# Performance work log

Measured on AMD Instinct MI355X. Metric: run time of the kernel, lower is better.

The kernel has to match this reference:

```python
import jax, jax.numpy as jnp
import numpy as np

H_HEADS = 16
D_K = 64
D_V = 64
D_MODEL = H_HEADS * D_K  # 1024
B, S = 2, 2048


def _xavier(key, shape):
    fan_in, fan_out = shape
    limit = float(np.sqrt(6.0 / (fan_in + fan_out)))
    return jax.random.uniform(key, shape, jnp.float32, -limit, limit)


def setup_inputs() -> dict:
    key = jax.random.key(0)
    ks = jax.random.split(key, 6)
    return {
        "batch": jax.random.normal(ks[0], (B, S, D_MODEL), jnp.float32),
        "attention_mask": jnp.zeros((S, S), jnp.float32),
        "W_Q": _xavier(ks[1], (D_MODEL, H_HEADS * D_K)),
        "W_K": _xavier(ks[2], (D_MODEL, H_HEADS * D_K)),
        "W_V": _xavier(ks[3], (D_MODEL, H_HEADS * D_V)),
        "b_Q": jnp.zeros((H_HEADS * D_K,), jnp.float32),
        "b_K": jnp.zeros((H_HEADS * D_K,), jnp.float32),
        "b_V": jnp.zeros((H_HEADS * D_V,), jnp.float32),
        "W_O": _xavier(ks[4], (H_HEADS * D_V, D_MODEL)),
        "b_O": jnp.zeros((D_MODEL,), jnp.float32),
    }


def reference(batch, attention_mask, W_Q, W_K, W_V, b_Q, b_K, b_V, W_O, b_O):
    # Batched equivalent of the per-head loop: project all heads at once,
    # then split the last dim into (h, d). Same math, one GEMM each.
    q = batch @ W_Q + b_Q  # [B,S,h*dk]
    k = batch @ W_K + b_K
    v = batch @ W_V + b_V
    q = q.reshape(B, S, H_HEADS, D_K)
    k = k.reshape(B, S, H_HEADS, D_K)
    v = v.reshape(B, S, H_HEADS, D_V)
    scale = 1.0 / jnp.sqrt(jnp.asarray(D_K, jnp.float32))
    scores = jnp.einsum("bqhd,bkhd->bhqk", q, k) * scale  # [B,h,S,S]
    scores = scores + attention_mask  # broadcast over batch & heads
    attn = jax.nn.softmax(scores, axis=-1)
    out = jnp.einsum("bhqk,bkhd->bqhd", attn, v)  # [B,S,h,dv]
    out = out.reshape(B, S, H_HEADS * D_V)  # concat over heads
    return out @ W_O + b_O
```

## Files before the change

kernel.cpp:

```cpp
#include <hip/hip_runtime.h>
#include <hip/hip_bf16.h>

typedef __attribute__((ext_vector_type(8))) short bf16x8;
typedef __attribute__((ext_vector_type(4))) float f32x4;
typedef __attribute__((ext_vector_type(4))) unsigned short u16x4;
typedef __attribute__((ext_vector_type(8))) unsigned short u16x8;

#define DEVI static __device__ __forceinline__

DEVI unsigned short f2bf(float f) {
  union { __hip_bfloat16 h; unsigned short u; } cv;
  cv.h = __float2bfloat16(f);
  return cv.u;
}

DEVI float bf2f(unsigned short u) {
  union { unsigned int i; float f; } cv;
  cv.i = (unsigned int)u << 16;
  return cv.f;
}

DEVI void gld_lds16(const unsigned short* g, unsigned short* l) {
  __builtin_amdgcn_global_load_lds(
      (const __attribute__((address_space(1))) unsigned int*)g,
      (__attribute__((address_space(3))) unsigned int*)l, 16, 0, 0);
}


__global__ void k_cvt_x(const float* __restrict__ x, unsigned short* __restrict__ xb) {
  int i = blockIdx.x * 256 + threadIdx.x;
  f32x4 v = *((const f32x4*)x + i);
  u16x4 o;
#pragma unroll
  for (int j = 0; j < 4; ++j) o[j] = f2bf(v[j]);
  *((u16x4*)xb + i) = o;
}

__global__ void k_wt(const float* __restrict__ Wq, const float* __restrict__ Wk,
                     const float* __restrict__ Wv, const float* __restrict__ Wo,
                     unsigned short* __restrict__ wqkvT, unsigned short* __restrict__ woT) {
  __shared__ float lt[32][33];
  int t = blockIdx.x;
  int g = t >> 10, r = t & 1023, kt = r >> 5, nt = r & 31;
  const float* W = (g == 0) ? Wq : (g == 1) ? Wk : (g == 2) ? Wv : Wo;
  unsigned short* out = (g < 3) ? (wqkvT + (size_t)g * 1024 * 1024) : woT;
  int tid = threadIdx.x;
  int row = tid >> 3, c4 = tid & 7;
  f32x4 v = *(const f32x4*)(W + (size_t)(kt * 32 + row) * 1024 + nt * 32 + c4 * 4);
#pragma unroll
  for (int j = 0; j < 4; ++j) lt[row][c4 * 4 + j] = v[j];
  __syncthreads();
  u16x4 o;
#pragma unroll
  for (int j = 0; j < 4; ++j) o[j] = f2bf(lt[c4 * 4 + j][row]);
  *(u16x4*)(out + (size_t)(nt * 32 + row) * 1024 + kt * 32 + c4 * 4) = o;
}

__global__ void k_bias(const float* __restrict__ bq, const float* __restrict__ bk,
                       const float* __restrict__ bv, float* __restrict__ bcat) {
  int i = blockIdx.x * 256 + threadIdx.x;
  if (i < 3072) bcat[i] = (i < 1024) ? bq[i] : (i < 2048) ? bk[i - 1024] : bv[i - 2048];
}

__global__ void k_mt(const float* __restrict__ mask, unsigned short* __restrict__ mU) {
  __shared__ float lt[32][33];
  int q0 = blockIdx.y * 32, k0 = blockIdx.x * 32;
  int tid = threadIdx.x;
  int row = tid >> 3, c4 = tid & 7;
  f32x4 v = *(const f32x4*)(mask + (size_t)(q0 + row) * 2048 + k0 + c4 * 4);
#pragma unroll
  for (int j = 0; j < 4; ++j) lt[row][c4 * 4 + j] = v[j] * 1.4426950408889634f;
  __syncthreads();
  int kq = tid >> 5, qr = tid & 31;
  u16x4 o;
#pragma unroll
  for (int j = 0; j < 4; ++j) o[j] = f2bf(lt[qr][kq * 4 + j]);
  *(u16x4*)(mU + ((size_t)(k0 >> 2) + kq) * 8192 + (size_t)(q0 + qr) * 4) = o;
}

__global__ void k_vt(const unsigned short* __restrict__ qkv, unsigned short* __restrict__ vt) {
  __shared__ unsigned short lt[64][72];
  int bh = blockIdx.y, s0 = blockIdx.x * 64;
  int b = bh >> 4, h = bh & 15;
  int tid = threadIdx.x;
#pragma unroll
  for (int i = 0; i < 2; ++i) {
    int c = tid + i * 256;
    int row = c >> 3, c8 = (c & 7) * 8;
    u16x8 v = *(const u16x8*)(qkv + (size_t)(b * 2048 + s0 + row) * 3072 + 2048 + h * 64 + c8);
#pragma unroll
    for (int j = 0; j < 8; ++j) lt[row][c8 + j] = v[j];
  }
  __syncthreads();
#pragma unroll
  for (int i = 0; i < 2; ++i) {
    int c = tid + i * 256;
    int d = c >> 3, s8 = (c & 7) * 8;
    u16x8 o;
#pragma unroll
    for (int j = 0; j < 8; ++j) o[j] = lt[s8 + j][d];
    *(u16x8*)(vt + (size_t)(bh * 64 + d) * 2048 + s0 + s8) = o;
  }
}

template <int OUT_BF16>
__launch_bounds__(256)
__global__ void k_gemm(const unsigned short* __restrict__ A,
                       const unsigned short* __restrict__ Bt,
                       const float* __restrict__ bias, void* __restrict__ C,
                       int M, int N, int K) {
  __shared__ unsigned short lA[128 * 32];
  __shared__ unsigned short lB[128 * 32];
  int tid = threadIdx.x;
  int m0 = blockIdx.y * 128, n0 = blockIdx.x * 128;
  int w = tid >> 6, l = tid & 63;
  int wm = (w >> 1) * 64, wn = (w & 1) * 64;
  int lg = l >> 4, lc = l & 15;
  f32x4 acc[4][4] = {};
  const unsigned short* Ab = A + (size_t)m0 * K;
  const unsigned short* Bb = Bt + (size_t)n0 * K;

  for (int kk = 0; kk < K; kk += 32) {
#pragma unroll
    for (int i = 0; i < 2; ++i) {
      int c = tid + i * 256;
      int row = c >> 2, c8 = (c & 3) * 8;
      gld_lds16(Ab + (size_t)row * K + kk + c8, lA + c * 8);
    }
#pragma unroll
    for (int i = 0; i < 2; ++i) {
      int c = tid + i * 256;
      int row = c >> 2, c8 = (c & 3) * 8;
      gld_lds16(Bb + (size_t)row * K + kk + c8, lB + c * 8);
    }
    __syncthreads();
    bf16x8 af[4], bfr[4];
#pragma unroll
    for (int mf = 0; mf < 4; ++mf)
      af[mf] = *(const bf16x8*)(lA + (wm + mf * 16 + lc) * 32 + lg * 8);
#pragma unroll
    for (int nf = 0; nf < 4; ++nf)
      bfr[nf] = *(const bf16x8*)(lB + (wn + nf * 16 + lc) * 32 + lg * 8);
#pragma unroll
    for (int mf = 0; mf < 4; ++mf)
#pragma unroll
      for (int nf = 0; nf < 4; ++nf)
        acc[mf][nf] = __builtin_amdgcn_mfma_f32_16x16x32_bf16(af[mf], bfr[nf], acc[mf][nf], 0, 0, 0);
    __syncthreads();
  }

  int lr = lg * 4;
  float bv[4];
#pragma unroll
  for (int nf = 0; nf < 4; ++nf) bv[nf] = bias[n0 + wn + nf * 16 + lc];
#pragma unroll
  for (int mf = 0; mf < 4; ++mf)
#pragma unroll
    for (int nf = 0; nf < 4; ++nf)
#pragma unroll
      for (int rr = 0; rr < 4; ++rr) {
        size_t gm = m0 + wm + mf * 16 + lr + rr;
        size_t gn = n0 + wn + nf * 16 + lc;
        float v = acc[mf][nf][rr] + bv[nf];
        if (OUT_BF16)
          ((unsigned short*)C)[gm * N + gn] = f2bf(v);
        else
          ((float*)C)[gm * N + gn] = v;
      }
}

__launch_bounds__(256, 4)
__global__ void k_attn(const unsigned short* __restrict__ qkv,
                       const unsigned short* __restrict__ vt,
                       const unsigned short* __restrict__ mU,
                       unsigned short* __restrict__ ao) {
  __shared__ unsigned short lK[2][64 * 64];
  __shared__ unsigned short lV[2][64 * 64];
  __shared__ unsigned short lP[64 * 64];
  int wg0 = blockIdx.x;
  int wg = (wg0 & 7) * 128 + (wg0 >> 3);
  int b = wg >> 9, r0 = wg & 511, h = r0 >> 5, qt = r0 & 31;
  int tid = threadIdx.x, w = tid >> 6, l = tid & 63;
  int lg = l >> 4, lc = l & 15;
  int c = lc & 7;
  int q0 = qt * 64 + w * 16;

  const unsigned short* Qb = qkv + (size_t)(b * 2048 + q0) * 3072 + h * 64;
  const unsigned short* Kb = qkv + (size_t)(b * 2048) * 3072 + 1024 + h * 64;
  const unsigned short* Vb = vt + (size_t)((b * 16 + h) * 64) * 2048;
  const unsigned short* mUb = mU + (size_t)lg * 8192 + (size_t)(q0 + lc) * 4;

  int rsub = l >> 3;
  int scol = ((l & 7) ^ rsub) * 8;

  bf16x8 qf[2];
#pragma unroll
  for (int ks = 0; ks < 2; ++ks)
    qf[ks] = *(const bf16x8*)(Qb + (size_t)lc * 3072 + ks * 32 + lg * 8);

  f32x4 o2[4] = {};
  float m = -1e30f, ll = 0.f;

#pragma unroll
  for (int i = 0; i < 2; ++i) {
    int r = i * 32 + w * 8 + rsub;
    gld_lds16(Kb + (size_t)r * 3072 + scol, &lK[0][(i * 4 + w) * 512]);
    gld_lds16(Vb + (size_t)r * 2048 + scol, &lV[0][(i * 4 + w) * 512]);
  }
  __syncthreads();

  int cur = 0;
  unsigned short* lPw = lP + (w * 16 + lc) * 64;
  for (int t = 0; t < 32; ++t) {
    int k0 = t * 64;
    if (t < 31) {
#pragma unroll
      for (int i = 0; i < 2; ++i) {
        int r = i * 32 + w * 8 + rsub;
        gld_lds16(Kb + (size_t)(k0 + 64 + r) * 3072 + scol, &lK[cur ^ 1][(i * 4 + w) * 512]);
        gld_lds16(Vb + (size_t)r * 2048 + k0 + 64 + scol, &lV[cur ^ 1][(i * 4 + w) * 512]);
      }
    }
    const unsigned short* lKc = lK[cur];
    const unsigned short* lVc = lV[cur];

    f32x4 s[4] = {};
#pragma unroll
    for (int ks = 0; ks < 2; ++ks) {
      bf16x8 kf[4];
#pragma unroll
      for (int blk = 0; blk < 4; ++blk)
        kf[blk] = *(const bf16x8*)(lKc + (blk * 16 + lc) * 64 +
                                   ((ks * 32 + lg * 8) ^ (c << 3)));
#pragma unroll
      for (int blk = 0; blk < 4; ++blk)
        s[blk] = __builtin_amdgcn_mfma_f32_16x16x32_bf16(kf[blk], qf[ks], s[blk], 0, 0, 0);
    }

    float tl[16];
#pragma unroll
    for (int blk = 0; blk < 4; ++blk) {
      u16x4 mv = *(const u16x4*)(mUb + ((size_t)(k0 >> 2) + blk * 4) * 8192);
#pragma unroll
      for (int rr = 0; rr < 4; ++rr)
        tl[blk * 4 + rr] = fmaf(s[blk][rr], 0.18033688011112042f, bf2f(mv[rr]));
    }

    float tm[8];
#pragma unroll
    for (int i = 0; i < 8; ++i) tm[i] = fmaxf(tl[2 * i], tl[2 * i + 1]);
#pragma unroll
    for (int i = 0; i < 4; ++i) tm[i] = fmaxf(tm[2 * i], tm[2 * i + 1]);
    float mx = fmaxf(fmaxf(tm[0], tm[1]), fmaxf(tm[2], tm[3]));
    mx = fmaxf(mx, __shfl_xor(mx, 16));
    mx = fmaxf(mx, __shfl_xor(mx, 32));
    float mn = fmaxf(m, mx);
    float al = exp2f(m - mn);
    m = mn;

    float psum = 0.f;
#pragma unroll
    for (int blk = 0; blk < 4; ++blk) {
      u16x4 pk;
#pragma unroll
      for (int rr = 0; rr < 4; ++rr) {
        float p = exp2f(tl[blk * 4 + rr] - mn);
        psum += p;
        pk[rr] = f2bf(p);
      }
      *(u16x4*)(lPw + (((blk * 32 + lg * 8) ^ (c << 4)) >> 1)) = pk;
    }
    ll = ll * al + psum;
#pragma unroll
    for (int nf = 0; nf < 4; ++nf)
#pragma unroll
      for (int rr = 0; rr < 4; ++rr) o2[nf][rr] *= al;

#pragma unroll
    for (int ks2 = 0; ks2 < 2; ++ks2) {
      bf16x8 pa = *(const bf16x8*)(lPw + (((ks2 * 64 + lg * 16) ^ (c << 4)) >> 1));
      bf16x8 vf[4];
#pragma unroll
      for (int nf = 0; nf < 4; ++nf)
        vf[nf] = *(const bf16x8*)(lVc + (nf * 16 + lc) * 64 +
                                  ((ks2 * 32 + lg * 8) ^ (c << 3)));
#pragma unroll
      for (int nf = 0; nf < 4; ++nf)
        o2[nf] = __builtin_amdgcn_mfma_f32_16x16x32_bf16(vf[nf], pa, o2[nf], 0, 0, 0);
    }

    __syncthreads();
    cur ^= 1;
  }

  ll += __shfl_xor(ll, 16);
  ll += __shfl_xor(ll, 32);
  float inv = 1.f / ll;
#pragma unroll
  for (int nf = 0; nf < 4; ++nf) {
    u16x4 pk;
#pragma unroll
    for (int rr = 0; rr < 4; ++rr) pk[rr] = f2bf(o2[nf][rr] * inv);
    *(u16x4*)(lPw + (((nf * 32 + lg * 8) ^ (c << 4)) >> 1)) = pk;
  }
  int rq = l >> 2, seg = l & 3, c2 = rq & 7;
  const unsigned short* lPr = lP + (w * 16 + rq) * 64;
#pragma unroll
  for (int half = 0; half < 2; ++half) {
    u16x8 ov = *(const u16x8*)(lPr + (((seg * 32 + half * 16) ^ (c2 << 4)) >> 1));
    *(u16x8*)(ao + (size_t)(b * 2048 + q0 + rq) * 1024 + h * 64 + seg * 16 + half * 8) = ov;
  }
}

extern "C" void kernel_launch(void* const* d_in, const int* in_sizes, int n_in,
                              void* d_out, int out_size, void* d_ws, size_t ws_size,
                              hipStream_t stream) {
  const float* batch = (const float*)d_in[0];
  const float* mask = (const float*)d_in[1];
  const float* Wq = (const float*)d_in[2];
  const float* Wk = (const float*)d_in[3];
  const float* Wv = (const float*)d_in[4];
  const float* bq = (const float*)d_in[5];
  const float* bk = (const float*)d_in[6];
  const float* bvv = (const float*)d_in[7];
  const float* Wo = (const float*)d_in[8];
  const float* bo = (const float*)d_in[9];

  char* ws = (char*)d_ws;
  unsigned short* Xb    = (unsigned short*)(ws);
  unsigned short* WqkvT = (unsigned short*)(ws + 8388608);
  unsigned short* WoT   = (unsigned short*)(ws + 14680064);
  float*          bcat  = (float*)(ws + 16777216);
  unsigned short* QKV   = (unsigned short*)(ws + 16789504);
  unsigned short* Vt    = (unsigned short*)(ws + 41955328);
  unsigned short* AO    = (unsigned short*)(ws + 50343936);
  unsigned short* mU    = Xb;

  hipLaunchKernelGGL(k_cvt_x, dim3(4096), dim3(256), 0, stream, batch, Xb);
  hipLaunchKernelGGL(k_wt, dim3(4096), dim3(256), 0, stream, Wq, Wk, Wv, Wo, WqkvT, WoT);
  hipLaunchKernelGGL(k_bias, dim3(12), dim3(256), 0, stream, bq, bk, bvv, bcat);
  hipLaunchKernelGGL((k_gemm<1>), dim3(24, 32), dim3(256), 0, stream,
                     Xb, WqkvT, bcat, (void*)QKV, 4096, 3072, 1024);
  hipLaunchKernelGGL(k_mt, dim3(64, 64), dim3(256), 0, stream, mask, mU);
  hipLaunchKernelGGL(k_vt, dim3(32, 32), dim3(256), 0, stream, QKV, Vt);
  hipLaunchKernelGGL(k_attn, dim3(1024), dim3(256), 0, stream, QKV, Vt, mU, AO);
  hipLaunchKernelGGL((k_gemm<0>), dim3(8, 32), dim3(256), 0, stream,
                     AO, WoT, bo, (void*)d_out, 4096, 1024, 1024);
}
```

Measured before the change: 260.0 us.

## Pre-pack K/V into MFMA fragment layout and load directly to registers in attention

The QKV GEMM now writes Q, K and V to separate planar buffers. A new pack kernel rearranges K and V into per-tile MFMA fragment order (V transposed), which lets the attention kernel load K/V straight from global memory into registers with register double-buffering, with no LDS staging and no per-tile barrier. It also adds a lazy softmax rescale that skips updating the running max unless it grows by more than 8 in log2 space, and raises wave priority around the MFMA blocks. The trade-offs are more register pressure and global-load latency exposed to the compute loop, and the lazy rescale adds a small numerical change.

```diff
diff --git a/kernel.cpp b/kernel.cpp
--- a/kernel.cpp
+++ b/kernel.cpp
@@ -78,32 +78,43 @@
   *(u16x4*)(mU + ((size_t)(k0 >> 2) + kq) * 8192 + (size_t)(q0 + qr) * 4) = o;
 }
 
-__global__ void k_vt(const unsigned short* __restrict__ qkv, unsigned short* __restrict__ vt) {
-  __shared__ unsigned short lt[64][72];
-  int bh = blockIdx.y, s0 = blockIdx.x * 64;
+__global__ void k_pack(const unsigned short* __restrict__ Ko,
+                       const unsigned short* __restrict__ Vo,
+                       unsigned short* __restrict__ Kp,
+                       unsigned short* __restrict__ Vp) {
+  __shared__ unsigned short lK[64][72], lV[64][72];
+  int t = blockIdx.x, bh = blockIdx.y;
   int b = bh >> 4, h = bh & 15;
   int tid = threadIdx.x;
-#pragma unroll
-  for (int i = 0; i < 2; ++i) {
-    int c = tid + i * 256;
-    int row = c >> 3, c8 = (c & 7) * 8;
-    u16x8 v = *(const u16x8*)(qkv + (size_t)(b * 2048 + s0 + row) * 3072 + 2048 + h * 64 + c8);
-#pragma unroll
-    for (int j = 0; j < 8; ++j) lt[row][c8 + j] = v[j];
+  int row = tid >> 2, seg = tid & 3;
+  size_t src = (size_t)(b * 2048 + t * 64 + row) * 1024 + h * 64 + seg * 16;
+#pragma unroll
+  for (int half = 0; half < 2; ++half) {
+    u16x8 kv = *(const u16x8*)(Ko + src + half * 8);
+    u16x8 vv = *(const u16x8*)(Vo + src + half * 8);
+#pragma unroll
+    for (int j = 0; j < 8; ++j) {
+      lK[row][seg * 16 + half * 8 + j] = kv[j];
+      lV[row][seg * 16 + half * 8 + j] = vv[j];
+    }
   }
   __syncthreads();
-#pragma unroll
-  for (int i = 0; i < 2; ++i) {
-    int c = tid + i * 256;
-    int d = c >> 3, s8 = (c & 7) * 8;
-    u16x8 o;
-#pragma unroll
-    for (int j = 0; j < 8; ++j) o[j] = lt[s8 + j][d];
-    *(u16x8*)(vt + (size_t)(bh * 64 + d) * 2048 + s0 + s8) = o;
-  }
-}
-
-template <int OUT_BF16>
+  int l = tid & 63, lg = l >> 4, lc = l & 15;
+  size_t outbase = ((size_t)bh * 32 + t) * 4096;
+#pragma unroll
+  for (int rep = 0; rep < 2; ++rep) {
+    int chunk = rep * 4 + (tid >> 6);
+    int hi = chunk >> 1, lo = chunk & 1;
+    u16x8 ko = *(const u16x8*)(&lK[hi * 16 + lc][lo * 32 + lg * 8]);
+    *(u16x8*)(Kp + outbase + chunk * 512 + l * 8) = ko;
+    u16x8 vo;
+#pragma unroll
+    for (int j = 0; j < 8; ++j) vo[j] = lV[lo * 32 + lg * 8 + j][hi * 16 + lc];
+    *(u16x8*)(Vp + outbase + chunk * 512 + l * 8) = vo;
+  }
+}
+
+template <int OUT_MODE>
 __launch_bounds__(256)
 __global__ void k_gemm(const unsigned short* __restrict__ A,
                        const unsigned short* __restrict__ Bt,
@@ -162,101 +173,95 @@
         size_t gm = m0 + wm + mf * 16 + lr + rr;
         size_t gn = n0 + wn + nf * 16 + lc;
         float v = acc[mf][nf][rr] + bv[nf];
-        if (OUT_BF16)
-          ((unsigned short*)C)[gm * N + gn] = f2bf(v);
+        if (OUT_MODE == 1)
+          ((unsigned short*)C)[(size_t)(gn >> 10) * 4194304 + gm * 1024 + (gn & 1023)] = f2bf(v);
         else
           ((float*)C)[gm * N + gn] = v;
       }
 }
 
 __launch_bounds__(256, 4)
-__global__ void k_attn(const unsigned short* __restrict__ qkv,
-                       const unsigned short* __restrict__ vt,
+__global__ void k_attn(const unsigned short* __restrict__ Qo,
+                       const unsigned short* __restrict__ Kp,
+                       const unsigned short* __restrict__ Vp,
                        const unsigned short* __restrict__ mU,
                        unsigned short* __restrict__ ao) {
-  __shared__ unsigned short lK[2][64 * 64];
-  __shared__ unsigned short lV[2][64 * 64];
   __shared__ unsigned short lP[64 * 64];
   int wg0 = blockIdx.x;
   int wg = (wg0 & 7) * 128 + (wg0 >> 3);
   int b = wg >> 9, r0 = wg & 511, h = r0 >> 5, qt = r0 & 31;
   int tid = threadIdx.x, w = tid >> 6, l = tid & 63;
-  int lg = l >> 4, lc = l & 15;
-  int c = lc & 7;
+  int lg = l >> 4, lc = l & 15, cb = lc & 7, l8 = l * 8;
   int q0 = qt * 64 + w * 16;
-
-  const unsigned short* Qb = qkv + (size_t)(b * 2048 + q0) * 3072 + h * 64;
-  const unsigned short* Kb = qkv + (size_t)(b * 2048) * 3072 + 1024 + h * 64;
-  const unsigned short* Vb = vt + (size_t)((b * 16 + h) * 64) * 2048;
+  int bh = b * 16 + h;
+
+  const unsigned short* Qb = Qo + (size_t)(b * 2048 + q0) * 1024 + h * 64;
+  const unsigned short* kp = Kp + (size_t)bh * 131072;
+  const unsigned short* vp = Vp + (size_t)bh * 131072;
   const unsigned short* mUb = mU + (size_t)lg * 8192 + (size_t)(q0 + lc) * 4;
-
-  int rsub = l >> 3;
-  int scol = ((l & 7) ^ rsub) * 8;
+  unsigned short* lPw = lP + (w * 16 + lc) * 64;
 
   bf16x8 qf[2];
 #pragma unroll
   for (int ks = 0; ks < 2; ++ks)
-    qf[ks] = *(const bf16x8*)(Qb + (size_t)lc * 3072 + ks * 32 + lg * 8);
+    qf[ks] = *(const bf16x8*)(Qb + (size_t)lc * 1024 + ks * 32 + lg * 8);
 
   f32x4 o2[4] = {};
   float m = -1e30f, ll = 0.f;
 
-#pragma unroll
-  for (int i = 0; i < 2; ++i) {
-    int r = i * 32 + w * 8 + rsub;
-    gld_lds16(Kb + (size_t)r * 3072 + scol, &lK[0][(i * 4 + w) * 512]);
-    gld_lds16(Vb + (size_t)r * 2048 + scol, &lV[0][(i * 4 + w) * 512]);
-  }
-  __syncthreads();
-
-  int cur = 0;
-  unsigned short* lPw = lP + (w * 16 + lc) * 64;
-  for (int t = 0; t < 32; ++t) {
-    int k0 = t * 64;
+  bf16x8 kA[8], kB[8];
+#pragma unroll
+  for (int c = 0; c < 8; ++c) kA[c] = *(const bf16x8*)(kp + c * 512 + l8);
+
+  auto body = [&](int t, bf16x8(&kc)[8], bf16x8(&kn)[8]) {
     if (t < 31) {
-#pragma unroll
-      for (int i = 0; i < 2; ++i) {
-        int r = i * 32 + w * 8 + rsub;
-        gld_lds16(Kb + (size_t)(k0 + 64 + r) * 3072 + scol, &lK[cur ^ 1][(i * 4 + w) * 512]);
-        gld_lds16(Vb + (size_t)r * 2048 + k0 + 64 + scol, &lV[cur ^ 1][(i * 4 + w) * 512]);
-      }
-    }
-    const unsigned short* lKc = lK[cur];
-    const unsigned short* lVc = lV[cur];
+      const unsigned short* kpt = kp + (size_t)(t + 1) * 4096;
+#pragma unroll
+      for (int c = 0; c < 8; ++c) kn[c] = *(const bf16x8*)(kpt + c * 512 + l8);
+    }
+    u16x4 mv[4];
+#pragma unroll
+    for (int blk = 0; blk < 4; ++blk)
+      mv[blk] = *(const u16x4*)(mUb + ((size_t)t * 16 + blk * 4) * 8192);
 
     f32x4 s[4] = {};
-#pragma unroll
-    for (int ks = 0; ks < 2; ++ks) {
-      bf16x8 kf[4];
+    __builtin_amdgcn_s_setprio(1);
+#pragma unroll
+    for (int ks = 0; ks < 2; ++ks)
 #pragma unroll
       for (int blk = 0; blk < 4; ++blk)
-        kf[blk] = *(const bf16x8*)(lKc + (blk * 16 + lc) * 64 +
-                                   ((ks * 32 + lg * 8) ^ (c << 3)));
-#pragma unroll
-      for (int blk = 0; blk < 4; ++blk)
-        s[blk] = __builtin_amdgcn_mfma_f32_16x16x32_bf16(kf[blk], qf[ks], s[blk], 0, 0, 0);
-    }
-
-    float tl[16];
-#pragma unroll
-    for (int blk = 0; blk < 4; ++blk) {
-      u16x4 mv = *(const u16x4*)(mUb + ((size_t)(k0 >> 2) + blk * 4) * 8192);
+        s[blk] = __builtin_amdgcn_mfma_f32_16x16x32_bf16(kc[blk * 2 + ks], qf[ks], s[blk], 0, 0, 0);
+    __builtin_amdgcn_s_setprio(0);
+
+    bf16x8 vb[8];
+    const unsigned short* vpt = vp + (size_t)t * 4096;
+#pragma unroll
+    for (int c = 0; c < 8; ++c) vb[c] = *(const bf16x8*)(vpt + c * 512 + l8);
+
+#pragma unroll
+    for (int blk = 0; blk < 4; ++blk)
 #pragma unroll
       for (int rr = 0; rr < 4; ++rr)
-        tl[blk * 4 + rr] = fmaf(s[blk][rr], 0.18033688011112042f, bf2f(mv[rr]));
-    }
-
-    float tm[8];
-#pragma unroll
-    for (int i = 0; i < 8; ++i) tm[i] = fmaxf(tl[2 * i], tl[2 * i + 1]);
-#pragma unroll
-    for (int i = 0; i < 4; ++i) tm[i] = fmaxf(tm[2 * i], tm[2 * i + 1]);
-    float mx = fmaxf(fmaxf(tm[0], tm[1]), fmaxf(tm[2], tm[3]));
+        s[blk][rr] = fmaf(s[blk][rr], 0.18033688011112042f, bf2f(mv[blk][rr]));
+
+    float t0 = fmaxf(fmaxf(s[0][0], s[0][1]), fmaxf(s[0][2], s[0][3]));
+    float t1 = fmaxf(fmaxf(s[1][0], s[1][1]), fmaxf(s[1][2], s[1][3]));
+    float t2 = fmaxf(fmaxf(s[2][0], s[2][1]), fmaxf(s[2][2], s[2][3]));
+    float t3 = fmaxf(fmaxf(s[3][0], s[3][1]), fmaxf(s[3][2], s[3][3]));
+    float mx = fmaxf(fmaxf(t0, t1), fmaxf(t2, t3));
     mx = fmaxf(mx, __shfl_xor(mx, 16));
     mx = fmaxf(mx, __shfl_xor(mx, 32));
-    float mn = fmaxf(m, mx);
-    float al = exp2f(m - mn);
-    m = mn;
+
+    if (!__all(mx <= m + 8.f)) {
+      float mn2 = fmaxf(m, mx);
+      float al = exp2f(m - mn2);
+      m = mn2;
+      ll *= al;
+#pragma unroll
+      for (int nf = 0; nf < 4; ++nf)
+#pragma unroll
+        for (int rr = 0; rr < 4; ++rr) o2[nf][rr] *= al;
+    }
 
     float psum = 0.f;
 #pragma unroll
@@ -264,33 +269,28 @@
       u16x4 pk;
 #pragma unroll
       for (int rr = 0; rr < 4; ++rr) {
-        float p = exp2f(tl[blk * 4 + rr] - mn);
+        float p = exp2f(s[blk][rr] - m);
         psum += p;
         pk[rr] = f2bf(p);
       }
-      *(u16x4*)(lPw + (((blk * 32 + lg * 8) ^ (c << 4)) >> 1)) = pk;
-    }
-    ll = ll * al + psum;
-#pragma unroll
-    for (int nf = 0; nf < 4; ++nf)
-#pragma unroll
-      for (int rr = 0; rr < 4; ++rr) o2[nf][rr] *= al;
+      *(u16x4*)(lPw + (((blk * 32 + lg * 8) ^ (cb << 4)) >> 1)) = pk;
+    }
+    ll += psum;
 
 #pragma unroll
     for (int ks2 = 0; ks2 < 2; ++ks2) {
-      bf16x8 pa = *(const bf16x8*)(lPw + (((ks2 * 64 + lg * 16) ^ (c << 4)) >> 1));
-      bf16x8 vf[4];
+      bf16x8 pa = *(const bf16x8*)(lPw + (((ks2 * 64 + lg * 16) ^ (cb << 4)) >> 1));
+      __builtin_amdgcn_s_setprio(1);
 #pragma unroll
       for (int nf = 0; nf < 4; ++nf)
-        vf[nf] = *(const bf16x8*)(lVc + (nf * 16 + lc) * 64 +
-                                  ((ks2 * 32 + lg * 8) ^ (c << 3)));
-#pragma unroll
-      for (int nf = 0; nf < 4; ++nf)
-        o2[nf] = __builtin_amdgcn_mfma_f32_16x16x32_bf16(vf[nf], pa, o2[nf], 0, 0, 0);
-    }
-
-    __syncthreads();
-    cur ^= 1;
+        o2[nf] = __builtin_amdgcn_mfma_f32_16x16x32_bf16(vb[nf * 2 + ks2], pa, o2[nf], 0, 0, 0);
+      __builtin_amdgcn_s_setprio(0);
+    }
+  };
+
+  for (int tt = 0; tt < 16; ++tt) {
+    body(2 * tt, kA, kB);
+    body(2 * tt + 1, kB, kA);
   }
 
   ll += __shfl_xor(ll, 16);
@@ -301,7 +301,7 @@
     u16x4 pk;
 #pragma unroll
     for (int rr = 0; rr < 4; ++rr) pk[rr] = f2bf(o2[nf][rr] * inv);
-    *(u16x4*)(lPw + (((nf * 32 + lg * 8) ^ (c << 4)) >> 1)) = pk;
+    *(u16x4*)(lPw + (((nf * 32 + lg * 8) ^ (cb << 4)) >> 1)) = pk;
   }
   int rq = l >> 2, seg = l & 3, c2 = rq & 7;
   const unsigned short* lPr = lP + (w * 16 + rq) * 64;
@@ -331,19 +331,22 @@
   unsigned short* WqkvT = (unsigned short*)(ws + 8388608);
   unsigned short* WoT   = (unsigned short*)(ws + 14680064);
   float*          bcat  = (float*)(ws + 16777216);
-  unsigned short* QKV   = (unsigned short*)(ws + 16789504);
-  unsigned short* Vt    = (unsigned short*)(ws + 41955328);
-  unsigned short* AO    = (unsigned short*)(ws + 50343936);
+  unsigned short* Qo    = (unsigned short*)(ws + 16789504);
+  unsigned short* Ko    = (unsigned short*)(ws + 25178112);
+  unsigned short* Vo    = (unsigned short*)(ws + 33566720);
+  unsigned short* Kp    = (unsigned short*)(ws + 41955328);
+  unsigned short* Vp    = (unsigned short*)(ws + 50343936);
   unsigned short* mU    = Xb;
+  unsigned short* AO    = Ko;
 
   hipLaunchKernelGGL(k_cvt_x, dim3(4096), dim3(256), 0, stream, batch, Xb);
   hipLaunchKernelGGL(k_wt, dim3(4096), dim3(256), 0, stream, Wq, Wk, Wv, Wo, WqkvT, WoT);
   hipLaunchKernelGGL(k_bias, dim3(12), dim3(256), 0, stream, bq, bk, bvv, bcat);
   hipLaunchKernelGGL((k_gemm<1>), dim3(24, 32), dim3(256), 0, stream,
-                     Xb, WqkvT, bcat, (void*)QKV, 4096, 3072, 1024);
+                     Xb, WqkvT, bcat, (void*)Qo, 4096, 3072, 1024);
   hipLaunchKernelGGL(k_mt, dim3(64, 64), dim3(256), 0, stream, mask, mU);
-  hipLaunchKernelGGL(k_vt, dim3(32, 32), dim3(256), 0, stream, QKV, Vt);
-  hipLaunchKernelGGL(k_attn, dim3(1024), dim3(256), 0, stream, QKV, Vt, mU, AO);
+  hipLaunchKernelGGL(k_pack, dim3(32, 32), dim3(256), 0, stream, Ko, Vo, Kp, Vp);
+  hipLaunchKernelGGL(k_attn, dim3(1024), dim3(256), 0, stream, Qo, Kp, Vp, mU, AO);
   hipLaunchKernelGGL((k_gemm<0>), dim3(8, 32), dim3(256), 0, stream,
                      AO, WoT, bo, (void*)d_out, 4096, 1024, 1024);
 }
```

After: 405.7 us. 56.1% more time.
